# Kernel optimization log

Measured on AMD Instinct MI355X. Metric: run time of the kernel, lower is better.

Reference implementation:

```python
import jax, jax.numpy as jnp
import numpy as np

N = 16384
IN_F = 256
OUT_F = 128
ALPHA = 0.2  # leaky relu negative slope
NEG = -9e15


def _xavier(key, shape, gain=1.414):
    fan_in, fan_out = shape
    a = gain * np.sqrt(6.0 / (fan_in + fan_out))
    return jax.random.uniform(key, shape, jnp.float32, -a, a)


def setup_inputs() -> dict:
    key = jax.random.key(0)
    k_h, k_adj, k_q, k_k, k_v = jax.random.split(key, 5)
    h = jax.random.normal(k_h, (N, IN_F), dtype=jnp.float32)
    adj = jax.random.randint(k_adj, (N, N), 0, 2, dtype=jnp.int32)
    W_query = _xavier(k_q, (IN_F, OUT_F))
    W_key = _xavier(k_k, (IN_F, OUT_F))
    W_value = _xavier(k_v, (IN_F, OUT_F))
    return {"h": h, "adj": adj, "W_query": W_query, "W_key": W_key, "W_value": W_value}


def reference(h, adj, W_query, W_key, W_value):
    # h: [N, in], adj: [N, N] 0/1
    Q = h @ W_query           # [N, out]
    K = h @ W_key             # [N, out]
    V = h @ W_value           # [N, out]
    e = jnp.einsum('nd,md->nm', Q, K)          # [N, N]
    e = jnp.where(e >= 0, e, ALPHA * e)         # leaky relu
    e = jnp.where(adj > 0, e, NEG)              # adjacency mask
    attention = jax.nn.softmax(e, axis=1)       # row softmax
    # dropout: eval mode (training=False) -> identity
    h_prime = attention @ V                     # [N, out]
    return jax.nn.elu(h_prime)                  # concat=True
```

## Files before the change

### kernel.cpp

```cpp
#include <hip/hip_runtime.h>

#define N_TOK 16384
#define ALPHA_LRELU 0.2f
#define NEGV -9e15f
#define NSPLIT 3
#define LOG2E 1.44269504f
#define DEFER_THR 8.0f

typedef _Float16 f16;
typedef __attribute__((ext_vector_type(8))) _Float16 f16x8;
typedef __attribute__((ext_vector_type(4))) float f32x4;
typedef __attribute__((ext_vector_type(4))) int i32x4;
typedef unsigned short u16;

__device__ __forceinline__ float bf2f(u16 b) {
  unsigned u = ((unsigned)b) << 16;
  return __builtin_bit_cast(float, u);
}
__device__ __forceinline__ f16x8 cvt8(i32x4 v) {
  f16x8 r;
#pragma unroll
  for (int i = 0; i < 4; ++i) {
    unsigned u = __builtin_bit_cast(unsigned, v[i]);
    r[2 * i]     = (f16)__builtin_bit_cast(float, (u & 0xffffu) << 16);
    r[2 * i + 1] = (f16)__builtin_bit_cast(float, u & 0xffff0000u);
  }
  return r;
}

__global__ __launch_bounds__(64) void detect_kernel(const u16* __restrict__ h16,
                                                    int* __restrict__ flag)
{
  int lane = threadIdx.x;
  unsigned u = h16[lane * 2];
  unsigned e = (u >> 7) & 0xFFu;
  int sane = (e >= 0x60u && e <= 0x8Eu) ? 1 : 0;
#pragma unroll
  for (int off = 32; off >= 1; off >>= 1) sane += __shfl_xor(sane, off);
  if (lane == 0) *flag = (sane >= 32) ? 1 : 0;
}

__global__ __launch_bounds__(256) void sentinel_kernel(float* __restrict__ out) {
  int i = blockIdx.x * 256 + threadIdx.x;
  if (i < N_TOK * 128) out[i] = 100.0f;
}

__global__ __launch_bounds__(256) void wt_kernel(
    const int* __restrict__ flag,
    const void* __restrict__ Wq, const void* __restrict__ Wk,
    const void* __restrict__ Wv, f16* __restrict__ Wt)
{
  const int isbf = *flag;
  int w = blockIdx.y;
  const void* W = (w == 0) ? Wq : (w == 1) ? Wk : Wv;
  int idx = blockIdx.x * 256 + threadIdx.x;
  int k = idx >> 7, n = idx & 127;
  float v = isbf ? bf2f(((const u16*)W)[idx]) : ((const float*)W)[idx];
  if (w == 0) v *= LOG2E;
  Wt[w * 32768 + n * 256 + k] = (f16)v;
}

__global__ __launch_bounds__(256) void qkv_kernel(
    const int* __restrict__ flag, const void* __restrict__ hvp,
    const f16* __restrict__ Wt,
    f16* __restrict__ Qo, f16* __restrict__ Ko, f16* __restrict__ Vt)
{
  const int isbf = *flag;
  const int mb = blockIdx.x * 64;
  const int gy = blockIdx.y;
  const int tid = threadIdx.x;
  const int wave = tid >> 6, lane = tid & 63, quad = lane >> 4, l16 = lane & 15;

  __shared__ __align__(16) f16 hs[64][256 + 8];

  if (isbf) {
    const u16* h = (const u16*)hvp;
#pragma unroll
    for (int i = 0; i < 8; ++i) {
      int c = i * 256 + tid;
      int r = c >> 5, o = c & 31;
      i32x4 v = *(const i32x4*)(h + (size_t)(mb + r) * 256 + o * 8);
      *(f16x8*)(&hs[r][o * 8]) = cvt8(v);
    }
  } else {
    const float* h = (const float*)hvp;
#pragma unroll
    for (int i = 0; i < 8; ++i) {
      int c = i * 256 + tid;
      int r = c >> 5, o = c & 31;
      const float* p = h + (size_t)(mb + r) * 256 + o * 8;
      f32x4 v0 = *(const f32x4*)p, v1 = *(const f32x4*)(p + 4);
      f16x8 q;
#pragma unroll
      for (int j = 0; j < 4; ++j) { q[j] = (f16)v0[j]; q[4 + j] = (f16)v1[j]; }
      *(f16x8*)(&hs[r][o * 8]) = q;
    }
  }
  __syncthreads();

  const f16* Wg = Wt + gy * 32768;

  if (gy < 2) {
    f16x8 a[8];
#pragma unroll
    for (int ks = 0; ks < 8; ++ks)
      a[ks] = *(const f16x8*)(&hs[wave * 16 + l16][ks * 32 + quad * 8]);
    f32x4 acc[8];
#pragma unroll
    for (int ct = 0; ct < 8; ++ct) acc[ct] = (f32x4){0.f, 0.f, 0.f, 0.f};
#pragma unroll
    for (int ks = 0; ks < 8; ++ks)
#pragma unroll
      for (int ct = 0; ct < 8; ++ct) {
        f16x8 b = *(const f16x8*)(Wg + (ct * 16 + l16) * 256 + ks * 32 + quad * 8);
        acc[ct] = __builtin_amdgcn_mfma_f32_16x16x32_f16(a[ks], b, acc[ct], 0, 0, 0);
      }
    f16* O = (gy == 0) ? Qo : Ko;
#pragma unroll
    for (int ct = 0; ct < 8; ++ct)
#pragma unroll
      for (int r = 0; r < 4; ++r)
        O[(size_t)(mb + wave * 16 + quad * 4 + r) * 128 + ct * 16 + l16] = (f16)acc[ct][r];
  } else {
    f32x4 acc[2][4];
#pragma unroll
    for (int ft = 0; ft < 2; ++ft)
#pragma unroll
      for (int bt = 0; bt < 4; ++bt) acc[ft][bt] = (f32x4){0.f, 0.f, 0.f, 0.f};
#pragma unroll
    for (int ks = 0; ks < 8; ++ks) {
      f16x8 a2[2], b2[4];
#pragma unroll
      for (int ft = 0; ft < 2; ++ft)
        a2[ft] = *(const f16x8*)(Wg + ((wave * 2 + ft) * 16 + l16) * 256 + ks * 32 + quad * 8);
#pragma unroll
      for (int bt = 0; bt < 4; ++bt)
        b2[bt] = *(const f16x8*)(&hs[bt * 16 + l16][ks * 32 + quad * 8]);
#pragma unroll
      for (int ft = 0; ft < 2; ++ft)
#pragma unroll
        for (int bt = 0; bt < 4; ++bt)
          acc[ft][bt] = __builtin_amdgcn_mfma_f32_16x16x32_f16(a2[ft], b2[bt], acc[ft][bt], 0, 0, 0);
    }
#pragma unroll
    for (int ft = 0; ft < 2; ++ft)
#pragma unroll
      for (int bt = 0; bt < 4; ++bt)
#pragma unroll
        for (int r = 0; r < 4; ++r)
          Vt[(size_t)((wave * 2 + ft) * 16 + quad * 4 + r) * N_TOK + mb + bt * 16 + l16] =
              (f16)acc[ft][bt][r];
  }
}

__global__ __launch_bounds__(256, 2) void flash_kernel(
    const f16* __restrict__ Q, const f16* __restrict__ Kg,
    const f16* __restrict__ Vt, const int* __restrict__ adj,
    float* __restrict__ Opart, float* __restrict__ mpart,
    float* __restrict__ lpart)
{
  const int qb = blockIdx.x * 64;
  const int ksec = blockIdx.y;
  const int base = 256 / NSPLIT;
  const int rem  = 256 % NSPLIT;
  const int iters = base + (ksec < rem ? 1 : 0);
  const int tile0 = ksec * base + (ksec < rem ? ksec : rem);
  const int kb0 = tile0 * 64;
  const int tid = threadIdx.x;
  const int wave = tid >> 6, lane = tid & 63, quad = lane >> 4, l16 = lane & 15;

  __shared__ __align__(16) f16 Ks[64][136];
  __shared__ __align__(16) f16 Vs[128][72];
  __shared__ __align__(16) f16 Ps[4][16][72];
  __shared__ __align__(8)  u16 As16[64][4];

  f16x8 qf[4];
#pragma unroll
  for (int ks = 0; ks < 4; ++ks)
    qf[ks] = *(const f16x8*)(Q + (size_t)(qb + wave * 16 + l16) * 128 + ks * 32 + quad * 8);

  f16x8 ONES;
#pragma unroll
  for (int j = 0; j < 8; ++j) ONES[j] = (f16)1.0f;

  const int shq = (l16 & 3) * 16 + (l16 >> 2);

  f32x4 Oacc[8];
#pragma unroll
  for (int ot = 0; ot < 8; ++ot) Oacc[ot] = (f32x4){0.f, 0.f, 0.f, 0.f};
  f32x4 Lacc = (f32x4){0.f, 0.f, 0.f, 0.f};
  float m2[4];
#pragma unroll
  for (int r = 0; r < 4; ++r) m2[r] = -INFINITY;

  i32x4 pK[4], pV[4], pA[4];
#pragma unroll
  for (int i = 0; i < 4; ++i) {
    int c = i * 256 + tid;
    pK[i] = *(const i32x4*)(Kg + (size_t)(kb0 + (c >> 4)) * 128 + (c & 15) * 8);
    pV[i] = *(const i32x4*)(Vt + (size_t)(c >> 3) * N_TOK + kb0 + (c & 7) * 8);
    pA[i] = *(const i32x4*)(adj + (size_t)(qb + (c >> 4)) * N_TOK + kb0 + (c & 15) * 4);
  }

  for (int it = 0; it < iters; ++it) {
    __syncthreads();
#pragma unroll
    for (int i = 0; i < 4; ++i) {
      int c = i * 256 + tid;
      *(f16x8*)(&Ks[c >> 4][(c & 15) * 8]) = __builtin_bit_cast(f16x8, pK[i]);
      *(f16x8*)(&Vs[c >> 3][(c & 7) * 8])  = __builtin_bit_cast(f16x8, pV[i]);
      unsigned long long b0 = __ballot(pA[i][0] > 0);
      unsigned long long b1 = __ballot(pA[i][1] > 0);
      unsigned long long b2 = __ballot(pA[i][2] > 0);
      unsigned long long b3 = __ballot(pA[i][3] > 0);
      if (lane < 16) {
        int j = lane & 3, g = lane >> 2;
        unsigned long long v = (j == 0) ? b0 : (j == 1) ? b1 : (j == 2) ? b2 : b3;
        As16[i * 16 + wave * 4 + g][j] = (u16)(v >> (16 * g));
      }
    }
    __syncthreads();
    if (it + 1 < iters) {
      int kb = kb0 + (it + 1) * 64;
#pragma unroll
      for (int i = 0; i < 4; ++i) {
        int c = i * 256 + tid;
        pK[i] = *(const i32x4*)(Kg + (size_t)(kb + (c >> 4)) * 128 + (c & 15) * 8);
        pV[i] = *(const i32x4*)(Vt + (size_t)(c >> 3) * N_TOK + kb + (c & 7) * 8);
        pA[i] = *(const i32x4*)(adj + (size_t)(qb + (c >> 4)) * N_TOK + kb + (c & 15) * 4);
      }
    }

    float sc[4][4];
#pragma unroll
    for (int ct = 0; ct < 4; ++ct) {
      f32x4 s = (f32x4){0.f, 0.f, 0.f, 0.f};
#pragma unroll
      for (int ks = 0; ks < 4; ++ks) {
        f16x8 b = *(const f16x8*)(&Ks[ct * 16 + l16][ks * 32 + quad * 8]);
        s = __builtin_amdgcn_mfma_f32_16x16x32_f16(qf[ks], b, s, 0, 0, 0);
      }
#pragma unroll
      for (int r = 0; r < 4; ++r) {
        float v = s[r];
        sc[ct][r] = fmaxf(v, ALPHA_LRELU * v);
      }
    }
#pragma unroll
    for (int r = 0; r < 4; ++r) {
      unsigned long long a64 =
          *(const unsigned long long*)(&As16[wave * 16 + quad * 4 + r][0]);
      unsigned y = (unsigned)(a64 >> shq);
#pragma unroll
      for (int ct = 0; ct < 4; ++ct)
        if (!((y >> (4 * ct)) & 1u)) sc[ct][r] = NEGV;
    }

    float mx[4];
#pragma unroll
    for (int r = 0; r < 4; ++r) {
      float m = fmaxf(fmaxf(sc[0][r], sc[1][r]), fmaxf(sc[2][r], sc[3][r]));
#pragma unroll
      for (int off = 8; off >= 1; off >>= 1)
        m = fmaxf(m, __shfl_xor(m, off, 16));
      mx[r] = m;
    }
    bool up = (mx[0] > m2[0] + DEFER_THR) | (mx[1] > m2[1] + DEFER_THR) |
              (mx[2] > m2[2] + DEFER_THR) | (mx[3] > m2[3] + DEFER_THR);
    if (__ballot(up)) {
      float al[4];
#pragma unroll
      for (int r = 0; r < 4; ++r) {
        float mn = fmaxf(m2[r], mx[r]);
        al[r] = exp2f(m2[r] - mn);
        m2[r] = mn;
      }
#pragma unroll
      for (int ot = 0; ot < 8; ++ot)
#pragma unroll
        for (int r = 0; r < 4; ++r) Oacc[ot][r] *= al[r];
#pragma unroll
      for (int r = 0; r < 4; ++r) Lacc[r] *= al[r];
    }

#pragma unroll
    for (int ct = 0; ct < 4; ++ct)
#pragma unroll
      for (int r = 0; r < 4; ++r)
        Ps[wave][quad * 4 + r][ct * 16 + l16] = (f16)exp2f(sc[ct][r] - m2[r]);

    asm volatile("s_waitcnt lgkmcnt(0)" ::: "memory");
    f16x8 pa0 = *(const f16x8*)(&Ps[wave][l16][quad * 8]);
    f16x8 pa1 = *(const f16x8*)(&Ps[wave][l16][32 + quad * 8]);
#pragma unroll
    for (int ot = 0; ot < 8; ++ot) {
      f16x8 b0 = *(const f16x8*)(&Vs[ot * 16 + l16][quad * 8]);
      f16x8 b1 = *(const f16x8*)(&Vs[ot * 16 + l16][32 + quad * 8]);
      Oacc[ot] = __builtin_amdgcn_mfma_f32_16x16x32_f16(pa0, b0, Oacc[ot], 0, 0, 0);
      Oacc[ot] = __builtin_amdgcn_mfma_f32_16x16x32_f16(pa1, b1, Oacc[ot], 0, 0, 0);
    }
    Lacc = __builtin_amdgcn_mfma_f32_16x16x32_f16(pa0, ONES, Lacc, 0, 0, 0);
    Lacc = __builtin_amdgcn_mfma_f32_16x16x32_f16(pa1, ONES, Lacc, 0, 0, 0);
  }

  float* Op = Opart + (size_t)ksec * (N_TOK * 128);
#pragma unroll
  for (int ot = 0; ot < 8; ++ot)
#pragma unroll
    for (int r = 0; r < 4; ++r) {
      int row = qb + wave * 16 + quad * 4 + r;
      Op[(size_t)row * 128 + ot * 16 + l16] = Oacc[ot][r];
    }
  if (l16 == 0) {
#pragma unroll
    for (int r = 0; r < 4; ++r) {
      int row = qb + wave * 16 + quad * 4 + r;
      mpart[ksec * N_TOK + row] = m2[r];
      lpart[ksec * N_TOK + row] = Lacc[r];
    }
  }
}

__global__ __launch_bounds__(256) void combine_kernel(
    const float* __restrict__ Opart, const float* __restrict__ mpart,
    const float* __restrict__ lpart, float* __restrict__ out)
{
  const int qb = blockIdx.x * 64;
  const int t = threadIdx.x;
  __shared__ float sa[NSPLIT][64], sdn[64];
  if (t < 64) {
    float m = -INFINITY;
#pragma unroll
    for (int s = 0; s < NSPLIT; ++s) m = fmaxf(m, mpart[s * N_TOK + qb + t]);
    float dn = 0.f;
#pragma unroll
    for (int s = 0; s < NSPLIT; ++s) {
      float a = exp2f(mpart[s * N_TOK + qb + t] - m);
      sa[s][t] = a;
      dn += lpart[s * N_TOK + qb + t] * a;
    }
    sdn[t] = 1.0f / dn;
  }
  __syncthreads();
  float* Og = out + (size_t)qb * 128;
#pragma unroll
  for (int i = 0; i < 8; ++i) {
    int idx = (i * 256 + t) * 4;
    int row = idx >> 7;
    f32x4 acc = (f32x4){0.f, 0.f, 0.f, 0.f};
#pragma unroll
    for (int s = 0; s < NSPLIT; ++s) {
      f32x4 o = *(const f32x4*)(Opart + (size_t)s * (N_TOK * 128) + (size_t)qb * 128 + idx);
      float a = sa[s][row];
#pragma unroll
      for (int j = 0; j < 4; ++j) acc[j] += o[j] * a;
    }
    float dn = sdn[row];
    f32x4 v;
#pragma unroll
    for (int j = 0; j < 4; ++j) {
      float x = acc[j] * dn;
      v[j] = (x > 0.f) ? x : (__expf(x) - 1.f);
    }
    *(f32x4*)(Og + idx) = v;
  }
}

__global__ __launch_bounds__(256) void flash1_kernel(
    const f16* __restrict__ Q, const f16* __restrict__ Kg,
    const f16* __restrict__ Vt, const int* __restrict__ adj,
    float* __restrict__ out)
{
  const int qb = blockIdx.x * 64;
  const int tid = threadIdx.x;
  const int wave = tid >> 6, lane = tid & 63, quad = lane >> 4, l16 = lane & 15;

  __shared__ __align__(16) f16 Ks[64][136];
  __shared__ __align__(16) f16 Vs[128][72];
  __shared__ __align__(16) int As[64][68];
  __shared__ __align__(16) f16 Ps[4][16][72];

  f16x8 qf[4];
#pragma unroll
  for (int ks = 0; ks < 4; ++ks)
    qf[ks] = *(const f16x8*)(Q + (size_t)(qb + wave * 16 + l16) * 128 + ks * 32 + quad * 8);
  f16x8 ONES;
#pragma unroll
  for (int j = 0; j < 8; ++j) ONES[j] = (f16)1.0f;

  f32x4 Oacc[8];
#pragma unroll
  for (int ot = 0; ot < 8; ++ot) Oacc[ot] = (f32x4){0.f, 0.f, 0.f, 0.f};
  f32x4 Lacc = (f32x4){0.f, 0.f, 0.f, 0.f};
  float m2[4];
#pragma unroll
  for (int r = 0; r < 4; ++r) m2[r] = -INFINITY;

  i32x4 pK[4], pV[4], pA[4];
#pragma unroll
  for (int i = 0; i < 4; ++i) {
    int c = i * 256 + tid;
    pK[i] = *(const i32x4*)(Kg + (size_t)(c >> 4) * 128 + (c & 15) * 8);
    pV[i] = *(const i32x4*)(Vt + (size_t)(c >> 3) * N_TOK + (c & 7) * 8);
    pA[i] = *(const i32x4*)(adj + (size_t)(qb + (c >> 4)) * N_TOK + (c & 15) * 4);
  }

  for (int it = 0; it < 256; ++it) {
    __syncthreads();
#pragma unroll
    for (int i = 0; i < 4; ++i) {
      int c = i * 256 + tid;
      *(f16x8*)(&Ks[c >> 4][(c & 15) * 8]) = __builtin_bit_cast(f16x8, pK[i]);
      *(f16x8*)(&Vs[c >> 3][(c & 7) * 8])  = __builtin_bit_cast(f16x8, pV[i]);
      *(i32x4*)(&As[c >> 4][(c & 15) * 4]) = pA[i];
    }
    __syncthreads();
    if (it + 1 < 256) {
      int kb = (it + 1) * 64;
#pragma unroll
      for (int i = 0; i < 4; ++i) {
        int c = i * 256 + tid;
        pK[i] = *(const i32x4*)(Kg + (size_t)(kb + (c >> 4)) * 128 + (c & 15) * 8);
        pV[i] = *(const i32x4*)(Vt + (size_t)(c >> 3) * N_TOK + kb + (c & 7) * 8);
        pA[i] = *(const i32x4*)(adj + (size_t)(qb + (c >> 4)) * N_TOK + kb + (c & 15) * 4);
      }
    }
    float sc[4][4];
#pragma unroll
    for (int ct = 0; ct < 4; ++ct) {
      f32x4 s = (f32x4){0.f, 0.f, 0.f, 0.f};
#pragma unroll
      for (int ks = 0; ks < 4; ++ks) {
        f16x8 b = *(const f16x8*)(&Ks[ct * 16 + l16][ks * 32 + quad * 8]);
        s = __builtin_amdgcn_mfma_f32_16x16x32_f16(qf[ks], b, s, 0, 0, 0);
      }
#pragma unroll
      for (int r = 0; r < 4; ++r) {
        float v = s[r];
        v = fmaxf(v, ALPHA_LRELU * v);
        sc[ct][r] = (As[wave * 16 + quad * 4 + r][ct * 16 + l16] > 0) ? v : NEGV;
      }
    }
    float mx[4];
#pragma unroll
    for (int r = 0; r < 4; ++r) {
      float m = fmaxf(fmaxf(sc[0][r], sc[1][r]), fmaxf(sc[2][r], sc[3][r]));
#pragma unroll
      for (int off = 8; off >= 1; off >>= 1)
        m = fmaxf(m, __shfl_xor(m, off, 16));
      mx[r] = m;
    }
    bool up = (mx[0] > m2[0] + DEFER_THR) | (mx[1] > m2[1] + DEFER_THR) |
              (mx[2] > m2[2] + DEFER_THR) | (mx[3] > m2[3] + DEFER_THR);
    if (__ballot(up)) {
      float al[4];
#pragma unroll
      for (int r = 0; r < 4; ++r) {
        float mn = fmaxf(m2[r], mx[r]);
        al[r] = exp2f(m2[r] - mn);
        m2[r] = mn;
      }
#pragma unroll
      for (int ot = 0; ot < 8; ++ot)
#pragma unroll
        for (int r = 0; r < 4; ++r) Oacc[ot][r] *= al[r];
#pragma unroll
      for (int r = 0; r < 4; ++r) Lacc[r] *= al[r];
    }
#pragma unroll
    for (int ct = 0; ct < 4; ++ct)
#pragma unroll
      for (int r = 0; r < 4; ++r)
        Ps[wave][quad * 4 + r][ct * 16 + l16] = (f16)exp2f(sc[ct][r] - m2[r]);

    asm volatile("s_waitcnt lgkmcnt(0)" ::: "memory");
    f16x8 pa0 = *(const f16x8*)(&Ps[wave][l16][quad * 8]);
    f16x8 pa1 = *(const f16x8*)(&Ps[wave][l16][32 + quad * 8]);
#pragma unroll
    for (int ot = 0; ot < 8; ++ot) {
      f16x8 b0 = *(const f16x8*)(&Vs[ot * 16 + l16][quad * 8]);
      f16x8 b1 = *(const f16x8*)(&Vs[ot * 16 + l16][32 + quad * 8]);
      Oacc[ot] = __builtin_amdgcn_mfma_f32_16x16x32_f16(pa0, b0, Oacc[ot], 0, 0, 0);
      Oacc[ot] = __builtin_amdgcn_mfma_f32_16x16x32_f16(pa1, b1, Oacc[ot], 0, 0, 0);
    }
    Lacc = __builtin_amdgcn_mfma_f32_16x16x32_f16(pa0, ONES, Lacc, 0, 0, 0);
    Lacc = __builtin_amdgcn_mfma_f32_16x16x32_f16(pa1, ONES, Lacc, 0, 0, 0);
  }
#pragma unroll
  for (int ot = 0; ot < 8; ++ot)
#pragma unroll
    for (int r = 0; r < 4; ++r) {
      float v = Oacc[ot][r] / Lacc[r];
      v = (v > 0.f) ? v : (__expf(v) - 1.f);
      int row = qb + wave * 16 + quad * 4 + r;
      out[(size_t)row * 128 + ot * 16 + l16] = v;
    }
}

extern "C" void kernel_launch(void* const* d_in, const int* in_sizes, int n_in,
                              void* d_out, int out_size, void* d_ws, size_t ws_size,
                              hipStream_t stream)
{
  const void* h  = d_in[0];
  const int* adj = (const int*)d_in[1];
  const void* Wq = d_in[2];
  const void* Wk = d_in[3];
  const void* Wv = d_in[4];
  float* out = (float*)d_out;

  char* ws = (char*)d_ws;
  int* flag = (int*)ws;
  f16* Wt = (f16*)(ws + 1024);
  f16* Q  = (f16*)(ws + 262144);
  f16* K  = (f16*)(ws + 4456448);
  f16* Vt = (f16*)(ws + 8650752);
  float* Opart = (float*)(ws + 12845056);
  float* mpart = (float*)(ws + 38010880);
  float* lpart = (float*)(ws + 38207488);
  const size_t NEED_BASE  = 12845056;
  const size_t NEED_SPLIT = 38404096;

  if (ws_size < NEED_BASE) {
    sentinel_kernel<<<(N_TOK * 128 + 255) / 256, 256, 0, stream>>>(out);
    return;
  }

  detect_kernel<<<1, 64, 0, stream>>>((const u16*)h, flag);
  wt_kernel<<<dim3(128, 3), 256, 0, stream>>>(flag, Wq, Wk, Wv, Wt);
  qkv_kernel<<<dim3(256, 3), 256, 0, stream>>>(flag, h, Wt, Q, K, Vt);

  if (ws_size >= NEED_SPLIT) {
    flash_kernel<<<dim3(256, NSPLIT), 256, 0, stream>>>(Q, K, Vt, adj,
                                                        Opart, mpart, lpart);
    combine_kernel<<<dim3(256), 256, 0, stream>>>(Opart, mpart, lpart, out);
  } else {
    flash1_kernel<<<dim3(256), 256, 0, stream>>>(Q, K, Vt, adj, out);
  }
}
```

Baseline: 1.598 ms.

## Double-buffer K/V in LDS and load adjacency mask directly per lane

Switches K and V shared-memory tiles to double buffers with a two-deep register prefetch, so each iteration needs only one barrier instead of two. The ballot-based bitmask packing of the adjacency tile through LDS is removed. Each lane instead loads its own adjacency ints for the next tile right after the score MFMAs. This cuts LDS traffic and synchronization, but the per-lane adjacency loads are strided 4-byte accesses and less coalesced, and the extra LDS usage may affect occupancy.

```diff
diff --git a/kernel.cpp b/kernel.cpp
--- a/kernel.cpp
+++ b/kernel.cpp
@@ -169,10 +169,9 @@
   const int tid = threadIdx.x;
   const int wave = tid >> 6, lane = tid & 63, quad = lane >> 4, l16 = lane & 15;
 
-  __shared__ __align__(16) f16 Ks[64][136];
-  __shared__ __align__(16) f16 Vs[128][72];
+  __shared__ __align__(16) f16 Ks[2][64][136];
+  __shared__ __align__(16) f16 Vs[2][128][72];
   __shared__ __align__(16) f16 Ps[4][16][72];
-  __shared__ __align__(8)  u16 As16[64][4];
 
   f16x8 qf[4];
 #pragma unroll
@@ -183,7 +182,10 @@
 #pragma unroll
   for (int j = 0; j < 8; ++j) ONES[j] = (f16)1.0f;
 
-  const int shq = (l16 & 3) * 16 + (l16 >> 2);
+  const int* aprow[4];
+#pragma unroll
+  for (int r = 0; r < 4; ++r)
+    aprow[r] = adj + (size_t)(qb + wave * 16 + quad * 4 + r) * N_TOK + l16;
 
   f32x4 Oacc[8];
 #pragma unroll
@@ -193,41 +195,56 @@
 #pragma unroll
   for (int r = 0; r < 4; ++r) m2[r] = -INFINITY;
 
-  i32x4 pK[4], pV[4], pA[4];
+  i32x4 pK[4], pV[4];
+  int am[4][4];
+
 #pragma unroll
   for (int i = 0; i < 4; ++i) {
     int c = i * 256 + tid;
     pK[i] = *(const i32x4*)(Kg + (size_t)(kb0 + (c >> 4)) * 128 + (c & 15) * 8);
     pV[i] = *(const i32x4*)(Vt + (size_t)(c >> 3) * N_TOK + kb0 + (c & 7) * 8);
-    pA[i] = *(const i32x4*)(adj + (size_t)(qb + (c >> 4)) * N_TOK + kb0 + (c & 15) * 4);
-  }
-
-  for (int it = 0; it < iters; ++it) {
-    __syncthreads();
+  }
+#pragma unroll
+  for (int r = 0; r < 4; ++r)
+#pragma unroll
+    for (int ct = 0; ct < 4; ++ct)
+      am[r][ct] = aprow[r][kb0 + ct * 16];
+#pragma unroll
+  for (int i = 0; i < 4; ++i) {
+    int c = i * 256 + tid;
+    *(f16x8*)(&Ks[0][c >> 4][(c & 15) * 8]) = __builtin_bit_cast(f16x8, pK[i]);
+    *(f16x8*)(&Vs[0][c >> 3][(c & 7) * 8])  = __builtin_bit_cast(f16x8, pV[i]);
+  }
+  if (iters > 1) {
+    int kb = kb0 + 64;
 #pragma unroll
     for (int i = 0; i < 4; ++i) {
       int c = i * 256 + tid;
-      *(f16x8*)(&Ks[c >> 4][(c & 15) * 8]) = __builtin_bit_cast(f16x8, pK[i]);
-      *(f16x8*)(&Vs[c >> 3][(c & 7) * 8])  = __builtin_bit_cast(f16x8, pV[i]);
-      unsigned long long b0 = __ballot(pA[i][0] > 0);
-      unsigned long long b1 = __ballot(pA[i][1] > 0);
-      unsigned long long b2 = __ballot(pA[i][2] > 0);
-      unsigned long long b3 = __ballot(pA[i][3] > 0);
-      if (lane < 16) {
-        int j = lane & 3, g = lane >> 2;
-        unsigned long long v = (j == 0) ? b0 : (j == 1) ? b1 : (j == 2) ? b2 : b3;
-        As16[i * 16 + wave * 4 + g][j] = (u16)(v >> (16 * g));
-      }
-    }
-    __syncthreads();
+      pK[i] = *(const i32x4*)(Kg + (size_t)(kb + (c >> 4)) * 128 + (c & 15) * 8);
+      pV[i] = *(const i32x4*)(Vt + (size_t)(c >> 3) * N_TOK + kb + (c & 7) * 8);
+    }
+  }
+  __syncthreads();
+
+  for (int it = 0; it < iters; ++it) {
+    const int cur = it & 1;
+    const int nxt = cur ^ 1;
+
     if (it + 1 < iters) {
-      int kb = kb0 + (it + 1) * 64;
+#pragma unroll
+      for (int i = 0; i < 4; ++i) {
+        int c = i * 256 + tid;
+        *(f16x8*)(&Ks[nxt][c >> 4][(c & 15) * 8]) = __builtin_bit_cast(f16x8, pK[i]);
+        *(f16x8*)(&Vs[nxt][c >> 3][(c & 7) * 8])  = __builtin_bit_cast(f16x8, pV[i]);
+      }
+    }
+    if (it + 2 < iters) {
+      int kb = kb0 + (it + 2) * 64;
 #pragma unroll
       for (int i = 0; i < 4; ++i) {
         int c = i * 256 + tid;
         pK[i] = *(const i32x4*)(Kg + (size_t)(kb + (c >> 4)) * 128 + (c & 15) * 8);
         pV[i] = *(const i32x4*)(Vt + (size_t)(c >> 3) * N_TOK + kb + (c & 7) * 8);
-        pA[i] = *(const i32x4*)(adj + (size_t)(qb + (c >> 4)) * N_TOK + kb + (c & 15) * 4);
       }
     }
 
@@ -237,23 +254,23 @@
       f32x4 s = (f32x4){0.f, 0.f, 0.f, 0.f};
 #pragma unroll
       for (int ks = 0; ks < 4; ++ks) {
-        f16x8 b = *(const f16x8*)(&Ks[ct * 16 + l16][ks * 32 + quad * 8]);
+        f16x8 b = *(const f16x8*)(&Ks[cur][ct * 16 + l16][ks * 32 + quad * 8]);
         s = __builtin_amdgcn_mfma_f32_16x16x32_f16(qf[ks], b, s, 0, 0, 0);
       }
 #pragma unroll
       for (int r = 0; r < 4; ++r) {
         float v = s[r];
-        sc[ct][r] = fmaxf(v, ALPHA_LRELU * v);
-      }
-    }
-#pragma unroll
-    for (int r = 0; r < 4; ++r) {
-      unsigned long long a64 =
-          *(const unsigned long long*)(&As16[wave * 16 + quad * 4 + r][0]);
-      unsigned y = (unsigned)(a64 >> shq);
-#pragma unroll
-      for (int ct = 0; ct < 4; ++ct)
-        if (!((y >> (4 * ct)) & 1u)) sc[ct][r] = NEGV;
+        v = fmaxf(v, ALPHA_LRELU * v);
+        sc[ct][r] = (am[r][ct] > 0) ? v : NEGV;
+      }
+    }
+    if (it + 1 < iters) {
+      int kb = kb0 + (it + 1) * 64;
+#pragma unroll
+      for (int r = 0; r < 4; ++r)
+#pragma unroll
+        for (int ct = 0; ct < 4; ++ct)
+          am[r][ct] = aprow[r][kb + ct * 16];
     }
 
     float mx[4];
@@ -294,13 +311,15 @@
     f16x8 pa1 = *(const f16x8*)(&Ps[wave][l16][32 + quad * 8]);
 #pragma unroll
     for (int ot = 0; ot < 8; ++ot) {
-      f16x8 b0 = *(const f16x8*)(&Vs[ot * 16 + l16][quad * 8]);
-      f16x8 b1 = *(const f16x8*)(&Vs[ot * 16 + l16][32 + quad * 8]);
+      f16x8 b0 = *(const f16x8*)(&Vs[cur][ot * 16 + l16][quad * 8]);
+      f16x8 b1 = *(const f16x8*)(&Vs[cur][ot * 16 + l16][32 + quad * 8]);
       Oacc[ot] = __builtin_amdgcn_mfma_f32_16x16x32_f16(pa0, b0, Oacc[ot], 0, 0, 0);
       Oacc[ot] = __builtin_amdgcn_mfma_f32_16x16x32_f16(pa1, b1, Oacc[ot], 0, 0, 0);
     }
     Lacc = __builtin_amdgcn_mfma_f32_16x16x32_f16(pa0, ONES, Lacc, 0, 0, 0);
     Lacc = __builtin_amdgcn_mfma_f32_16x16x32_f16(pa1, ONES, Lacc, 0, 0, 0);
+
+    __syncthreads();
   }
 
   float* Op = Opart + (size_t)ksec * (N_TOK * 128);
```

Result: faster. 1.537 ms (-3.8%).
